# Kernel tuning notes

Measured on AMD Instinct MI355X. Metric: run time of the kernel, lower is better.

Reference implementation:

```python
import jax, jax.numpy as jnp
import numpy as np
import math

D_MODEL, N_HEADS, D_FF = 1024, 16, 4096
D_K = D_MODEL // N_HEADS
B, S = 4, 2048
EPS = 1e-5


def layer_norm(x, gamma, beta):
    mean = jnp.mean(x, axis=-1, keepdims=True)
    var = jnp.mean((x - mean) ** 2, axis=-1, keepdims=True)  # unbiased=False
    return gamma * (x - mean) / jnp.sqrt(var + EPS) + beta


def setup_inputs() -> dict:
    key = jax.random.key(0)
    ks = jax.random.split(key, 7)
    std_attn = math.sqrt(2.0 / (D_MODEL + D_MODEL))
    std_ff1 = math.sqrt(2.0 / (D_MODEL + D_FF))
    std_ff2 = math.sqrt(2.0 / (D_FF + D_MODEL))
    return {
        "x": jax.random.normal(ks[0], (B, S, D_MODEL), jnp.float32),
        "W_q": jax.random.normal(ks[1], (D_MODEL, D_MODEL), jnp.float32) * std_attn,
        "W_k": jax.random.normal(ks[2], (D_MODEL, D_MODEL), jnp.float32) * std_attn,
        "W_v": jax.random.normal(ks[3], (D_MODEL, D_MODEL), jnp.float32) * std_attn,
        "W_o": jax.random.normal(ks[4], (D_MODEL, D_MODEL), jnp.float32) * std_attn,
        "W1": jax.random.normal(ks[5], (D_MODEL, D_FF), jnp.float32) * std_ff1,
        "b1": jnp.zeros((D_FF,), jnp.float32),
        "W2": jax.random.normal(ks[6], (D_FF, D_MODEL), jnp.float32) * std_ff2,
        "b2": jnp.zeros((D_MODEL,), jnp.float32),
        "ln1_gamma": jnp.ones((D_MODEL,), jnp.float32),
        "ln1_beta": jnp.zeros((D_MODEL,), jnp.float32),
        "ln2_gamma": jnp.ones((D_MODEL,), jnp.float32),
        "ln2_beta": jnp.zeros((D_MODEL,), jnp.float32),
    }


def reference(x, W_q, W_k, W_v, W_o, W1, b1, W2, b2,
              ln1_gamma, ln1_beta, ln2_gamma, ln2_beta):
    b, s, d = x.shape
    # pre-LN attention block
    ln1 = layer_norm(x, ln1_gamma, ln1_beta)
    q = (ln1 @ W_q).reshape(b, s, N_HEADS, D_K)
    k = (ln1 @ W_k).reshape(b, s, N_HEADS, D_K)
    v = (ln1 @ W_v).reshape(b, s, N_HEADS, D_K)
    scores = jnp.einsum("bqhd,bkhd->bhqk", q, k) / math.sqrt(D_K)
    attn = jax.nn.softmax(scores, axis=-1)
    ctx = jnp.einsum("bhqk,bkhd->bqhd", attn, v).reshape(b, s, d)
    attn_out = ctx @ W_o
    attn_residual = x + attn_out
    # pre-LN FFN block
    ln2 = layer_norm(attn_residual, ln2_gamma, ln2_beta)
    ff = jax.nn.relu(ln2 @ W1 + b1) @ W2 + b2
    return attn_residual + ff
```

## Files before the change

### kernel.cpp

```cpp
#include <hip/hip_runtime.h>
#include <hip/hip_bf16.h>

typedef __attribute__((ext_vector_type(4)))  float  floatx4;
typedef __attribute__((ext_vector_type(16))) float  floatx16;
typedef __attribute__((ext_vector_type(8)))  short  shortx8;
typedef __attribute__((ext_vector_type(4)))  short  shortx4;

__device__ __forceinline__ short f2bf(float f) {
    unsigned u = __float_as_uint(f);
    u += 0x7fffu + ((u >> 16) & 1u);
    return (short)(u >> 16);
}
__device__ __forceinline__ float bf2f(short s) {
    return __uint_as_float(((unsigned)(unsigned short)s) << 16);
}
__device__ __forceinline__ float fast_exp2(float x) {
#if __has_builtin(__builtin_amdgcn_exp2f)
    return __builtin_amdgcn_exp2f(x);
#else
    return exp2f(x);
#endif
}

__device__ __forceinline__ void load_lds16(const void* g, void* l) {
    __builtin_amdgcn_global_load_lds(
        (const __attribute__((address_space(1))) unsigned int*)g,
        (__attribute__((address_space(3))) unsigned int*)l,
        16, 0, 0);
}

__global__ __launch_bounds__(256)
void transpose_w(const float* __restrict__ src, short* __restrict__ dst, int K, int N)
{
    __shared__ __align__(16) float tile[32][33];
    const int n0 = blockIdx.x * 32, k0 = blockIdx.y * 32;
    const int tx = threadIdx.x & 31, ty = threadIdx.x >> 5;
    for (int i = 0; i < 32; i += 8)
        tile[ty + i][tx] = src[(size_t)(k0 + ty + i) * N + n0 + tx];
    __syncthreads();
    for (int i = 0; i < 32; i += 8)
        dst[(size_t)(n0 + ty + i) * K + k0 + tx] = f2bf(tile[tx][ty + i]);
}

__global__ __launch_bounds__(256)
void ln_bf16(const float* __restrict__ x, const float* __restrict__ g,
             const float* __restrict__ be, short* __restrict__ out)
{
    const int row = blockIdx.x;
    const int tid = threadIdx.x;
    const float4 v = reinterpret_cast<const float4*>(x + (size_t)row * 1024)[tid];
    float s  = v.x + v.y + v.z + v.w;
    float ss = v.x * v.x + v.y * v.y + v.z * v.z + v.w * v.w;
    for (int off = 32; off > 0; off >>= 1) {
        s  += __shfl_down(s,  off);
        ss += __shfl_down(ss, off);
    }
    __shared__ float rs[4], rss[4];
    const int wave = tid >> 6, lane = tid & 63;
    if (lane == 0) { rs[wave] = s; rss[wave] = ss; }
    __syncthreads();
    const float S    = rs[0] + rs[1] + rs[2] + rs[3];
    const float SS   = rss[0] + rss[1] + rss[2] + rss[3];
    const float mean = S * (1.0f / 1024.0f);
    const float var  = SS * (1.0f / 1024.0f) - mean * mean;
    const float rstd = rsqrtf(var + 1e-5f);
    const float4 gg = reinterpret_cast<const float4*>(g)[tid];
    const float4 bb = reinterpret_cast<const float4*>(be)[tid];
    shortx4 o;
    o[0] = f2bf(gg.x * ((v.x - mean) * rstd) + bb.x);
    o[1] = f2bf(gg.y * ((v.y - mean) * rstd) + bb.y);
    o[2] = f2bf(gg.z * ((v.z - mean) * rstd) + bb.z);
    o[3] = f2bf(gg.w * ((v.w - mean) * rstd) + bb.w);
    *reinterpret_cast<shortx4*>(out + (size_t)row * 1024 + tid * 4) = o;
}

__device__ __forceinline__ floatx4 mfma2(shortx8 a0, shortx8 a1,
                                         shortx8 b0, shortx8 b1, floatx4 c) {
    c = __builtin_amdgcn_mfma_f32_16x16x32_bf16(a0, b0, c, 0, 0, 0);
    return __builtin_amdgcn_mfma_f32_16x16x32_bf16(a1, b1, c, 0, 0, 0);
}

template <int EPI>
__global__ __launch_bounds__(512, 2)
void gemm256(const short* __restrict__ A, const short* __restrict__ Bt,
             short* __restrict__ Cb, float* __restrict__ Cf,
             const float* __restrict__ bias, const float* __restrict__ resid,
             int M, int N, int K, int tilesN)
{
    extern __shared__ __align__(16) short lds[];
    short* const As0 = lds;
    short* const Bs0 = lds + 16384;
    short* const As1 = lds + 32768;
    short* const Bs1 = lds + 49152;

    int wg = blockIdx.x;
    {
        const int nwg = gridDim.x;
        const int q = nwg >> 3, r = nwg & 7;
        const int xcd = wg & 7, loc = wg >> 3;
        wg = (xcd < r ? xcd * (q + 1) : r * (q + 1) + (xcd - r) * q) + loc;
    }
    const int tm = wg / tilesN, tn = wg - tm * tilesN;
    const size_t bm = (size_t)tm * 256, bn = (size_t)tn * 256;

    const int tid  = threadIdx.x;
    const int wave = tid >> 6;
    const int lane = tid & 63;
    const int quad = lane >> 4;
    const int l16  = lane & 15;
    const int wm   = wave >> 2;
    const int wn   = wave & 3;

    const int x7  = l16 & 7;
    const int go0 = ((quad    ) ^ x7) * 8;
    const int go1 = ((quad + 4) ^ x7) * 8;
    const int aoff = (wm * 128 + l16) * 64;
    const int boff = (wn *  64 + l16) * 64;

    const int rcall = tid >> 3;
    const int gl    = (tid & 7) ^ (rcall & 7);
    const short* srcA = A  + (bm + rcall) * (size_t)K + gl * 8;
    const short* srcB = Bt + (bn + rcall) * (size_t)K + gl * 8;
    const int dstw = wave * 512;

#define STG(dst, src, c, k0) \
    load_lds16((src) + (size_t)(c) * 64 * K + (k0), (dst) + (c) * 4096 + dstw)

    const int NT = K >> 6;

    STG(As0, srcA, 0, 0); STG(As0, srcA, 2, 0);
    STG(Bs0, srcB, 0, 0); STG(Bs0, srcB, 1, 0);
    STG(Bs0, srcB, 2, 0); STG(Bs0, srcB, 3, 0);
    STG(As0, srcA, 1, 0); STG(As0, srcA, 3, 0);

    floatx4 acc[8][4];
#pragma unroll
    for (int i = 0; i < 8; i++)
#pragma unroll
        for (int j = 0; j < 4; j++)
            acc[i][j] = (floatx4){0.f, 0.f, 0.f, 0.f};

    asm volatile("s_waitcnt vmcnt(2)" ::: "memory");
    __builtin_amdgcn_s_barrier();

    for (int t = 0; t < NT; ++t) {
        const short* Asc = (t & 1) ? As1 : As0;
        const short* Bsc = (t & 1) ? Bs1 : Bs0;
        short* Asn = (t & 1) ? As0 : As1;
        short* Bsn = (t & 1) ? Bs0 : Bs1;
        const int kn = (t + 1) << 6;
        const bool pf = (t + 1) < NT;

        shortx8 aF[4][2], bF[2][2];

#pragma unroll
        for (int mi = 0; mi < 4; ++mi) {
            aF[mi][0] = *(const shortx8*)&Asc[aoff + mi * 1024 + go0];
            aF[mi][1] = *(const shortx8*)&Asc[aoff + mi * 1024 + go1];
        }
#pragma unroll
        for (int ni = 0; ni < 2; ++ni) {
            bF[ni][0] = *(const shortx8*)&Bsc[boff + ni * 1024 + go0];
            bF[ni][1] = *(const shortx8*)&Bsc[boff + ni * 1024 + go1];
        }
        if (pf) { STG(Asn, srcA, 0, kn); STG(Asn, srcA, 2, kn); }
        __builtin_amdgcn_s_barrier();
        asm volatile("s_waitcnt lgkmcnt(0)" ::: "memory");
        __builtin_amdgcn_s_setprio(1);
#pragma unroll
        for (int mi = 0; mi < 4; ++mi)
#pragma unroll
            for (int ni = 0; ni < 2; ++ni)
                acc[mi][ni] = mfma2(aF[mi][0], aF[mi][1], bF[ni][0], bF[ni][1], acc[mi][ni]);
        __builtin_amdgcn_s_setprio(0);
        __builtin_amdgcn_s_barrier();

#pragma unroll
        for (int ni = 0; ni < 2; ++ni) {
            bF[ni][0] = *(const shortx8*)&Bsc[boff + (ni + 2) * 1024 + go0];
            bF[ni][1] = *(const shortx8*)&Bsc[boff + (ni + 2) * 1024 + go1];
        }
        if (pf) { STG(Bsn, srcB, 0, kn); STG(Bsn, srcB, 1, kn); }
        __builtin_amdgcn_s_barrier();
        asm volatile("s_waitcnt lgkmcnt(0)" ::: "memory");
        __builtin_amdgcn_s_setprio(1);
#pragma unroll
        for (int mi = 0; mi < 4; ++mi)
#pragma unroll
            for (int ni = 0; ni < 2; ++ni)
                acc[mi][ni + 2] = mfma2(aF[mi][0], aF[mi][1], bF[ni][0], bF[ni][1], acc[mi][ni + 2]);
        __builtin_amdgcn_s_setprio(0);
        if (pf) asm volatile("s_waitcnt vmcnt(4)" ::: "memory");
        else    asm volatile("s_waitcnt vmcnt(0)" ::: "memory");
        __builtin_amdgcn_s_barrier();

#pragma unroll
        for (int mi = 0; mi < 4; ++mi) {
            aF[mi][0] = *(const shortx8*)&Asc[aoff + (mi + 4) * 1024 + go0];
            aF[mi][1] = *(const shortx8*)&Asc[aoff + (mi + 4) * 1024 + go1];
        }
        if (pf) { STG(Bsn, srcB, 2, kn); STG(Bsn, srcB, 3, kn); }
        __builtin_amdgcn_s_barrier();
        asm volatile("s_waitcnt lgkmcnt(0)" ::: "memory");
        __builtin_amdgcn_s_setprio(1);
#pragma unroll
        for (int mi = 0; mi < 4; ++mi)
#pragma unroll
            for (int ni = 0; ni < 2; ++ni)
                acc[mi + 4][ni + 2] = mfma2(aF[mi][0], aF[mi][1], bF[ni][0], bF[ni][1], acc[mi + 4][ni + 2]);
        __builtin_amdgcn_s_setprio(0);
        __builtin_amdgcn_s_barrier();

#pragma unroll
        for (int ni = 0; ni < 2; ++ni) {
            bF[ni][0] = *(const shortx8*)&Bsc[boff + ni * 1024 + go0];
            bF[ni][1] = *(const shortx8*)&Bsc[boff + ni * 1024 + go1];
        }
        if (pf) { STG(Asn, srcA, 1, kn); STG(Asn, srcA, 3, kn); }
        __builtin_amdgcn_s_barrier();
        asm volatile("s_waitcnt lgkmcnt(0)" ::: "memory");
        __builtin_amdgcn_s_setprio(1);
#pragma unroll
        for (int mi = 0; mi < 4; ++mi)
#pragma unroll
            for (int ni = 0; ni < 2; ++ni)
                acc[mi + 4][ni] = mfma2(aF[mi][0], aF[mi][1], bF[ni][0], bF[ni][1], acc[mi + 4][ni]);
        __builtin_amdgcn_s_setprio(0);
        asm volatile("s_waitcnt vmcnt(2)" ::: "memory");
        __builtin_amdgcn_s_barrier();
    }
#undef STG

#pragma unroll
    for (int mi = 0; mi < 8; ++mi) {
#pragma unroll
        for (int ni = 0; ni < 4; ++ni) {
            const size_t row0 = bm + wm * 128 + mi * 16 + quad * 4;
            const size_t col  = bn + wn * 64 + ni * 16 + l16;
#pragma unroll
            for (int r = 0; r < 4; ++r) {
                float v = acc[mi][ni][r];
                const size_t idx = (row0 + r) * (size_t)N + col;
                if (EPI == 0) {
                    Cb[idx] = f2bf(v);
                } else if (EPI == 1) {
                    v += bias[col];
                    Cb[idx] = f2bf(v > 0.f ? v : 0.f);
                } else if (EPI == 2) {
                    Cf[idx] = resid[idx] + v;
                } else {
                    v += bias[col];
                    Cf[idx] = resid[idx] + v;
                }
            }
        }
    }
}

__global__ __launch_bounds__(256)
void transpose_v(const short* __restrict__ qkv, short* __restrict__ vt)
{
    __shared__ __align__(16) short tile[64][65];
    const int st = blockIdx.x, h = blockIdx.y, b = blockIdx.z;
    const int t = threadIdx.x;
    for (int i = 0; i < 2; i++) {
        const int idx = i * 256 + t;
        const int s = idx >> 3, dg = idx & 7;
        shortx8 val = *(const shortx8*)&qkv[(size_t)(b * 2048 + st * 64 + s) * 3072
                                           + 2048 + h * 64 + dg * 8];
        for (int u = 0; u < 8; u++) tile[s][dg * 8 + u] = val[u];
    }
    __syncthreads();
    const int d = t >> 2, sg = (t & 3) * 16;
    shortx8 lo, hi;
    for (int i = 0; i < 8; i++) {
        lo[i] = tile[sg + i][d];
        hi[i] = tile[sg + 8 + i][d];
    }
    const size_t base = ((size_t)(b * 16 + h) * 64 + d) * 2048 + st * 64 + sg;
    *(shortx8*)&vt[base]     = lo;
    *(shortx8*)&vt[base + 8] = hi;
}

__global__ __launch_bounds__(512, 4)
void attention_kernel(const short* __restrict__ qkv, const short* __restrict__ vt,
                      short* __restrict__ ctx)
{
    const int qt = blockIdx.x, h = blockIdx.y, b = blockIdx.z;
    const int tid  = threadIdx.x;
    const int wave = tid >> 6;
    const int lane = tid & 63;
    const int l32  = lane & 31;
    const int hf   = lane >> 5;

    __shared__ __align__(16) short Ks[64 * 72];
    __shared__ __align__(16) short Vs[64 * 72];
    __shared__ __align__(16) short Ps[8][32 * 72];

    const int q0 = qt * 256 + wave * 32;
    const float qscale = 0.125f * 1.44269504088896f;
    const short* qrow = qkv + (size_t)(b * 2048 + q0 + l32) * 3072 + h * 64;
    shortx8 qf[4];
    for (int dk = 0; dk < 4; dk++) {
        shortx8 raw = *(const shortx8*)&qrow[dk * 16 + hf * 8];
        for (int j = 0; j < 8; j++) raw[j] = f2bf(bf2f(raw[j]) * qscale);
        qf[dk] = raw;
    }

    floatx16 accO[2];
    for (int t = 0; t < 2; t++)
        for (int r = 0; r < 16; r++) accO[t][r] = 0.f;
    float lsum = 0.f;

    const short* kbase = qkv + (size_t)(b * 2048) * 3072 + 1024 + h * 64;
    const short* vbase = vt + ((size_t)(b * 16 + h) * 64) * 2048;
    short* const psw = &Ps[wave][0];
    unsigned* const pswd = (unsigned*)psw;

    const int ss = tid >> 3, sdg = tid & 7;

    for (int kt = 0; kt < 32; ++kt) {
        __syncthreads();
        {
            shortx8 kv = *(const shortx8*)&kbase[(size_t)(kt * 64 + ss) * 3072 + sdg * 8];
            *(shortx8*)&Ks[ss * 72 + sdg * 8] = kv;
            shortx8 vv = *(const shortx8*)&vbase[(size_t)ss * 2048 + kt * 64 + sdg * 8];
            *(shortx8*)&Vs[ss * 72 + sdg * 8] = vv;
        }
        __syncthreads();

        for (int t = 0; t < 2; t++) {
            floatx16 c;
            for (int r = 0; r < 16; r++) c[r] = 0.f;
            for (int dk = 0; dk < 4; dk++) {
                shortx8 kf = *(const shortx8*)&Ks[(t * 32 + l32) * 72 + dk * 16 + hf * 8];
                c = __builtin_amdgcn_mfma_f32_32x32x16_bf16(kf, qf[dk], c, 0, 0, 0);
            }
            for (int R = 0; R < 4; R++) {
                float2 a, bb;
                a.x  = fast_exp2(c[4 * R + 0]);
                a.y  = fast_exp2(c[4 * R + 1]);
                bb.x = fast_exp2(c[4 * R + 2]);
                bb.y = fast_exp2(c[4 * R + 3]);
                lsum += (a.x + a.y) + (bb.x + bb.y);
                union { __hip_bfloat162 h2[2]; uint2 u; } pk;
                pk.h2[0] = __float22bfloat162_rn(a);
                pk.h2[1] = __float22bfloat162_rn(bb);
                *(uint2*)&pswd[l32 * 36 + t * 16 + 4 * R + 2 * hf] = pk.u;
            }
        }
        asm volatile("s_waitcnt lgkmcnt(0)" ::: "memory");

        shortx8 pf[4];
        for (int sk = 0; sk < 4; sk++)
            pf[sk] = *(const shortx8*)&psw[l32 * 72 + sk * 16 + hf * 8];

        for (int t = 0; t < 2; t++) {
            floatx16 c = accO[t];
            for (int sk = 0; sk < 4; sk++) {
                shortx8 vf = *(const shortx8*)&Vs[(t * 32 + l32) * 72 + sk * 16 + hf * 8];
                c = __builtin_amdgcn_mfma_f32_32x32x16_bf16(vf, pf[sk], c, 0, 0, 0);
            }
            accO[t] = c;
        }
    }

    const float lfull = lsum + __shfl_xor(lsum, 32);
    const float inv = 1.0f / lfull;
    const size_t crow = (size_t)(b * 2048 + q0 + l32) * 1024 + h * 64;
    for (int t = 0; t < 2; t++)
        for (int R = 0; R < 4; R++) {
            float2 a, bb;
            a.x  = accO[t][4 * R + 0] * inv;
            a.y  = accO[t][4 * R + 1] * inv;
            bb.x = accO[t][4 * R + 2] * inv;
            bb.y = accO[t][4 * R + 3] * inv;
            union { __hip_bfloat162 h2[2]; uint2 u; } pk;
            pk.h2[0] = __float22bfloat162_rn(a);
            pk.h2[1] = __float22bfloat162_rn(bb);
            *(uint2*)&ctx[crow + t * 32 + 8 * R + 4 * hf] = pk.u;
        }
}

extern "C" void kernel_launch(void* const* d_in, const int* in_sizes, int n_in,
                              void* d_out, int out_size, void* d_ws, size_t ws_size,
                              hipStream_t stream)
{
    const float* x   = (const float*)d_in[0];
    const float* Wq  = (const float*)d_in[1];
    const float* Wk  = (const float*)d_in[2];
    const float* Wv  = (const float*)d_in[3];
    const float* Wo  = (const float*)d_in[4];
    const float* W1  = (const float*)d_in[5];
    const float* b1  = (const float*)d_in[6];
    const float* W2  = (const float*)d_in[7];
    const float* b2  = (const float*)d_in[8];
    const float* g1  = (const float*)d_in[9];
    const float* be1 = (const float*)d_in[10];
    const float* g2  = (const float*)d_in[11];
    const float* be2 = (const float*)d_in[12];
    float* out = (float*)d_out;
    char*  ws  = (char*)d_ws;

    const size_t MiB = 1u << 20;
    short* regA   = (short*)(ws);
    short* qkv    = (short*)(ws + 16 * MiB);
    short* vt     = (short*)(ws + 64 * MiB);
    short* ff1    = qkv;
    short* Wqkv_t = (short*)(ws + 80 * MiB);
    short* Wo_t   = (short*)(ws + 86 * MiB);
    short* W1_t   = (short*)(ws + 88 * MiB);
    short* W2_t   = (short*)(ws + 96 * MiB);

    const dim3 blk(256);
    const unsigned LDSB = 131072;

    static int attr_once = []() {
        hipFuncSetAttribute(reinterpret_cast<const void*>(gemm256<0>),
                            hipFuncAttributeMaxDynamicSharedMemorySize, 131072);
        hipFuncSetAttribute(reinterpret_cast<const void*>(gemm256<1>),
                            hipFuncAttributeMaxDynamicSharedMemorySize, 131072);
        hipFuncSetAttribute(reinterpret_cast<const void*>(gemm256<2>),
                            hipFuncAttributeMaxDynamicSharedMemorySize, 131072);
        hipFuncSetAttribute(reinterpret_cast<const void*>(gemm256<3>),
                            hipFuncAttributeMaxDynamicSharedMemorySize, 131072);
        return 0;
    }();
    (void)attr_once;

    transpose_w<<<dim3(32, 32),  blk, 0, stream>>>(Wq, Wqkv_t,                  1024, 1024);
    transpose_w<<<dim3(32, 32),  blk, 0, stream>>>(Wk, Wqkv_t + 1024 * 1024,    1024, 1024);
    transpose_w<<<dim3(32, 32),  blk, 0, stream>>>(Wv, Wqkv_t + 2 * 1024 * 1024,1024, 1024);
    transpose_w<<<dim3(32, 32),  blk, 0, stream>>>(Wo, Wo_t,                    1024, 1024);
    transpose_w<<<dim3(128, 32), blk, 0, stream>>>(W1, W1_t,                    1024, 4096);
    transpose_w<<<dim3(32, 128), blk, 0, stream>>>(W2, W2_t,                    4096, 1024);

    ln_bf16<<<8192, blk, 0, stream>>>(x, g1, be1, regA);
    gemm256<0><<<dim3(384), dim3(512), LDSB, stream>>>(regA, Wqkv_t, qkv, nullptr,
                                                       nullptr, nullptr, 8192, 3072, 1024, 12);
    transpose_v<<<dim3(32, 16, 4), blk, 0, stream>>>(qkv, vt);
    attention_kernel<<<dim3(8, 16, 4), dim3(512), 0, stream>>>(qkv, vt, regA);
    gemm256<2><<<dim3(128), dim3(512), LDSB, stream>>>(regA, Wo_t, nullptr, out,
                                                       nullptr, x, 8192, 1024, 1024, 4);
    ln_bf16<<<8192, blk, 0, stream>>>(out, g2, be2, regA);
    gemm256<1><<<dim3(512), dim3(512), LDSB, stream>>>(regA, W1_t, ff1, nullptr,
                                                       b1, nullptr, 8192, 4096, 1024, 16);
    gemm256<3><<<dim3(128), dim3(512), LDSB, stream>>>(ff1, W2_t, nullptr, out,
                                                       b2, out, 8192, 1024, 4096, 4);
}
```

Baseline: 552.3 us.

## Split-K the FFN2 GEMM with atomic accumulation and batch all prefetch loads

Adds a split-K option to the GEMM. The K=4096 FFN down-projection now runs as 2 splits over 256 workgroups instead of 128, and results are accumulated into the output with float atomicAdd, with the bias added only by split 0. The point is to fill more of the CUs on this small-grid GEMM. The next tile's global-to-LDS loads are also all issued at the start of each iteration rather than spread across the four sub-phases, with the wait count adjusted to match. The costs are atomic traffic on the output, results that are no longer bit-deterministic, and a prefetch pattern that may cause more contention in the other GEMMs.

New measurement: 561.3 us. No clear change (+1.6%).

```diff
diff --git a/kernel.cpp b/kernel.cpp
--- a/kernel.cpp
+++ b/kernel.cpp
@@ -85,7 +85,7 @@
 void gemm256(const short* __restrict__ A, const short* __restrict__ Bt,
              short* __restrict__ Cb, float* __restrict__ Cf,
              const float* __restrict__ bias, const float* __restrict__ resid,
-             int M, int N, int K, int tilesN)
+             int M, int N, int K, int tilesN, int nsplit)
 {
     extern __shared__ __align__(16) short lds[];
     short* const As0 = lds;
@@ -100,8 +100,13 @@
         const int xcd = wg & 7, loc = wg >> 3;
         wg = (xcd < r ? xcd * (q + 1) : r * (q + 1) + (xcd - r) * q) + loc;
     }
-    const int tm = wg / tilesN, tn = wg - tm * tilesN;
+    const int ntiles = gridDim.x / nsplit;
+    const int sp   = wg / ntiles;
+    const int tile = wg - sp * ntiles;
+    const int tm = tile / tilesN, tn = tile - tm * tilesN;
     const size_t bm = (size_t)tm * 256, bn = (size_t)tn * 256;
+    const int Ks   = K / nsplit;
+    const int kbeg = sp * Ks;
 
     const int tid  = threadIdx.x;
     const int wave = tid >> 6;
@@ -119,14 +124,14 @@
 
     const int rcall = tid >> 3;
     const int gl    = (tid & 7) ^ (rcall & 7);
-    const short* srcA = A  + (bm + rcall) * (size_t)K + gl * 8;
-    const short* srcB = Bt + (bn + rcall) * (size_t)K + gl * 8;
+    const short* srcA = A  + (bm + rcall) * (size_t)K + kbeg + gl * 8;
+    const short* srcB = Bt + (bn + rcall) * (size_t)K + kbeg + gl * 8;
     const int dstw = wave * 512;
 
 #define STG(dst, src, c, k0) \
     load_lds16((src) + (size_t)(c) * 64 * K + (k0), (dst) + (c) * 4096 + dstw)
 
-    const int NT = K >> 6;
+    const int NT = Ks >> 6;
 
     STG(As0, srcA, 0, 0); STG(As0, srcA, 2, 0);
     STG(Bs0, srcB, 0, 0); STG(Bs0, srcB, 1, 0);
@@ -163,7 +168,12 @@
             bF[ni][0] = *(const shortx8*)&Bsc[boff + ni * 1024 + go0];
             bF[ni][1] = *(const shortx8*)&Bsc[boff + ni * 1024 + go1];
         }
-        if (pf) { STG(Asn, srcA, 0, kn); STG(Asn, srcA, 2, kn); }
+        if (pf) {
+            STG(Asn, srcA, 0, kn); STG(Asn, srcA, 2, kn);
+            STG(Bsn, srcB, 0, kn); STG(Bsn, srcB, 1, kn);
+            STG(Bsn, srcB, 2, kn); STG(Bsn, srcB, 3, kn);
+            STG(Asn, srcA, 1, kn); STG(Asn, srcA, 3, kn);
+        }
         __builtin_amdgcn_s_barrier();
         asm volatile("s_waitcnt lgkmcnt(0)" ::: "memory");
         __builtin_amdgcn_s_setprio(1);
@@ -180,7 +190,6 @@
             bF[ni][0] = *(const shortx8*)&Bsc[boff + (ni + 2) * 1024 + go0];
             bF[ni][1] = *(const shortx8*)&Bsc[boff + (ni + 2) * 1024 + go1];
         }
-        if (pf) { STG(Bsn, srcB, 0, kn); STG(Bsn, srcB, 1, kn); }
         __builtin_amdgcn_s_barrier();
         asm volatile("s_waitcnt lgkmcnt(0)" ::: "memory");
         __builtin_amdgcn_s_setprio(1);
@@ -190,7 +199,7 @@
             for (int ni = 0; ni < 2; ++ni)
                 acc[mi][ni + 2] = mfma2(aF[mi][0], aF[mi][1], bF[ni][0], bF[ni][1], acc[mi][ni + 2]);
         __builtin_amdgcn_s_setprio(0);
-        if (pf) asm volatile("s_waitcnt vmcnt(4)" ::: "memory");
+        if (pf) asm volatile("s_waitcnt vmcnt(8)" ::: "memory");
         else    asm volatile("s_waitcnt vmcnt(0)" ::: "memory");
         __builtin_amdgcn_s_barrier();
 
@@ -199,7 +208,6 @@
             aF[mi][0] = *(const shortx8*)&Asc[aoff + (mi + 4) * 1024 + go0];
             aF[mi][1] = *(const shortx8*)&Asc[aoff + (mi + 4) * 1024 + go1];
         }
-        if (pf) { STG(Bsn, srcB, 2, kn); STG(Bsn, srcB, 3, kn); }
         __builtin_amdgcn_s_barrier();
         asm volatile("s_waitcnt lgkmcnt(0)" ::: "memory");
         __builtin_amdgcn_s_setprio(1);
@@ -216,7 +224,6 @@
             bF[ni][0] = *(const shortx8*)&Bsc[boff + ni * 1024 + go0];
             bF[ni][1] = *(const shortx8*)&Bsc[boff + ni * 1024 + go1];
         }
-        if (pf) { STG(Asn, srcA, 1, kn); STG(Asn, srcA, 3, kn); }
         __builtin_amdgcn_s_barrier();
         asm volatile("s_waitcnt lgkmcnt(0)" ::: "memory");
         __builtin_amdgcn_s_setprio(1);
@@ -248,9 +255,12 @@
                     Cb[idx] = f2bf(v > 0.f ? v : 0.f);
                 } else if (EPI == 2) {
                     Cf[idx] = resid[idx] + v;
-                } else {
+                } else if (EPI == 3) {
                     v += bias[col];
                     Cf[idx] = resid[idx] + v;
+                } else {
+                    if (sp == 0) v += bias[col];
+                    atomicAdd(&Cf[idx], v);
                 }
             }
         }
@@ -422,7 +432,7 @@
                             hipFuncAttributeMaxDynamicSharedMemorySize, 131072);
         hipFuncSetAttribute(reinterpret_cast<const void*>(gemm256<2>),
                             hipFuncAttributeMaxDynamicSharedMemorySize, 131072);
-        hipFuncSetAttribute(reinterpret_cast<const void*>(gemm256<3>),
+        hipFuncSetAttribute(reinterpret_cast<const void*>(gemm256<4>),
                             hipFuncAttributeMaxDynamicSharedMemorySize, 131072);
         return 0;
     }();
@@ -437,14 +447,14 @@
 
     ln_bf16<<<8192, blk, 0, stream>>>(x, g1, be1, regA);
     gemm256<0><<<dim3(384), dim3(512), LDSB, stream>>>(regA, Wqkv_t, qkv, nullptr,
-                                                       nullptr, nullptr, 8192, 3072, 1024, 12);
+                                                       nullptr, nullptr, 8192, 3072, 1024, 12, 1);
     transpose_v<<<dim3(32, 16, 4), blk, 0, stream>>>(qkv, vt);
     attention_kernel<<<dim3(8, 16, 4), dim3(512), 0, stream>>>(qkv, vt, regA);
     gemm256<2><<<dim3(128), dim3(512), LDSB, stream>>>(regA, Wo_t, nullptr, out,
-                                                       nullptr, x, 8192, 1024, 1024, 4);
+                                                       nullptr, x, 8192, 1024, 1024, 4, 1);
     ln_bf16<<<8192, blk, 0, stream>>>(out, g2, be2, regA);
     gemm256<1><<<dim3(512), dim3(512), LDSB, stream>>>(regA, W1_t, ff1, nullptr,
-                                                       b1, nullptr, 8192, 4096, 1024, 16);
-    gemm256<3><<<dim3(128), dim3(512), LDSB, stream>>>(ff1, W2_t, nullptr, out,
-                                                       b2, out, 8192, 1024, 4096, 4);
-}
+                                                       b1, nullptr, 8192, 4096, 1024, 16, 1);
+    gemm256<4><<<dim3(256), dim3(512), LDSB, stream>>>(ff1, W2_t, nullptr, out,
+                                                       b2, nullptr, 8192, 1024, 4096, 4, 2);
+}
```
